# Performance work log

Measured on AMD Instinct MI355X. Metric: run time of the kernel, lower is better.

## Reference

```python
import jax, jax.numpy as jnp
import numpy as np

D = 1024      # d_model
H = 16        # heads
KD = 64       # per-head dim
STRIDE = 64   # local chunk size
LH = 8        # local heads
GH = H - LH   # global heads
C = 4         # attended positions per global head per chunk


def setup_inputs() -> dict:
    key = jax.random.key(0)
    ks = jax.random.split(key, 12)
    B, S = 4, 4096
    sc = 1.0 / np.sqrt(D)
    x = jax.random.normal(ks[0], (B, S, D), jnp.float32)
    input_mask = jax.random.randint(ks[1], (B, S), 0, 2).astype(bool)
    Wq = jax.random.normal(ks[2], (D, D), jnp.float32) * sc
    bq = jax.random.normal(ks[3], (D,), jnp.float32) * 0.01
    Wk = jax.random.normal(ks[4], (D, D), jnp.float32) * sc
    bk = jax.random.normal(ks[5], (D,), jnp.float32) * 0.01
    Wv = jax.random.normal(ks[6], (D, D), jnp.float32) * sc
    bv = jax.random.normal(ks[7], (D,), jnp.float32) * 0.01
    Wo = jax.random.normal(ks[8], (D, D), jnp.float32) * sc
    bo = jax.random.normal(ks[9], (D,), jnp.float32) * 0.01
    return {"x": x, "input_mask": input_mask, "Wq": Wq, "bq": bq,
            "Wk": Wk, "bk": bk, "Wv": Wv, "bv": bv, "Wo": Wo, "bo": bo}


def reference(x, input_mask, Wq, bq, Wk, bk, Wv, bv, Wo, bo):
    B, S, _ = x.shape
    q = (x @ Wq.T + bq).reshape(B, S, H, KD)
    k = (x @ Wk.T + bk).reshape(B, S, H, KD)
    v = (x @ Wv.T + bv).reshape(B, S, H, KD)

    # ---- local heads: per the original code, the local attention scores are
    # computed but discarded; local_qkv = chunk_local_value reshaped back,
    # which is exactly the (head-major) local values. We reproduce that math.
    local_qkv = jnp.transpose(v[:, :, :LH, :], (0, 2, 1, 3))  # (B, LH, S, KD)

    # ---- global heads: each global head attends, inside every chunk, to a
    # fixed window of C positions near the end of the chunk.
    nc = S // STRIDE
    start = STRIDE - GH * C
    base = jnp.arange(start, STRIDE).reshape(GH, C)          # (GH, C)
    offs = jnp.arange(0, S, STRIDE)                          # (nc,)
    idx = (base[:, None, :] + offs[None, :, None]).reshape(GH, nc * C)  # (GH, L)
    L = nc * C

    gq = jnp.transpose(q[:, :, LH:, :], (0, 2, 1, 3))        # (B, GH, S, KD)
    gk = jnp.transpose(k[:, :, LH:, :], (0, 2, 1, 3))
    gv = jnp.transpose(v[:, :, LH:, :], (0, 2, 1, 3))

    h_idx = jnp.arange(GH)[:, None]                          # (GH, 1)
    gk_sel = gk[:, h_idx, idx, :]                            # (B, GH, L, KD)
    gv_sel = gv[:, h_idx, idx, :]                            # (B, GH, L, KD)

    qk = jnp.einsum('bhsd,bhld->bhsl', gq, gk_sel) * (KD ** -0.5)
    gmask = input_mask[:, idx]                               # (B, GH, L)
    qk = jnp.where(gmask[:, :, None, :], jnp.float32(-1e10), qk)
    attn = jax.nn.softmax(qk, axis=-1)
    g_out = jnp.einsum('bhsl,bhld->bhsd', attn, gv_sel)      # (B, GH, S, KD)

    qkv = jnp.concatenate([local_qkv, g_out], axis=1)        # (B, H, S, KD)
    qkv = jnp.transpose(qkv, (0, 2, 1, 3)).reshape(B, S, H * KD)
    return qkv @ Wo.T + bo
```

## Files before the change

kernel.cpp:

```cpp
#include <hip/hip_runtime.h>
#include <stdint.h>


typedef __bf16 bf16_t;
typedef __bf16 bf16x4 __attribute__((ext_vector_type(4)));
typedef __bf16 bf16x8 __attribute__((ext_vector_type(8)));
typedef float floatx4 __attribute__((ext_vector_type(4)));

#define MFMA16(a, b, c) __builtin_amdgcn_mfma_f32_16x16x32_bf16((a), (b), (c), 0, 0, 0)

__device__ __forceinline__ void glds16(const bf16_t* g, const bf16_t* lds_base) {
  __builtin_amdgcn_global_load_lds(
      (const __attribute__((address_space(1))) uint32_t*)(uintptr_t)g,
      (__attribute__((address_space(3))) uint32_t*)(uintptr_t)lds_base, 16, 0, 0);
}

#define VMCNT(n)  asm volatile("s_waitcnt vmcnt(" #n ")" ::: "memory")
#define LGKMCNT0  asm volatile("s_waitcnt lgkmcnt(0)" ::: "memory")
#define SBAR      __builtin_amdgcn_s_barrier()
#define SCHED0    __builtin_amdgcn_sched_barrier(0)

__global__ void cvt_f32_bf16(const float* __restrict__ src, bf16_t* __restrict__ dst, int n) {
  const int i = (blockIdx.x * 256 + threadIdx.x) * 4;
  if (i < n) {
    float4 v = *(const float4*)(src + i);
    bf16x4 d = {(bf16_t)v.x, (bf16_t)v.y, (bf16_t)v.z, (bf16_t)v.w};
    *(bf16x4*)(dst + i) = d;
  }
}

__global__ void pack_bias(const float* __restrict__ bv, const float* __restrict__ bq,
                          const float* __restrict__ bk, float* __restrict__ bcat) {
  const int i = blockIdx.x * 256 + threadIdx.x;
  float v;
  if (i < 1024) v = bv[i];
  else if (i < 1536) v = bq[i - 512];
  else v = bk[i - 1024];
  bcat[i] = v;
}

#define G8_DECL                                                                 \
  __shared__ bf16_t As[2][16384];                                               \
  __shared__ bf16_t Bs[2][16384];                                               \
  const int tid = threadIdx.x;                                                  \
  const int w = tid >> 6, l = tid & 63;                                         \
  const int lq = l >> 4, lm = l & 15;                                           \
  const int wr = (w >> 2) << 7;                      \
  const int wc = (w & 3) << 6;                \
  floatx4 acc[8][4];                                                            \
  { floatx4 z = {0.f, 0.f, 0.f, 0.f};                                           \
    _Pragma("unroll") for (int i = 0; i < 8; ++i)                               \
    _Pragma("unroll") for (int j = 0; j < 4; ++j) acc[i][j] = z; }              \
  const int t7 = tid & 127, t8 = tid >> 7;                                      \
  const int sbase = ((((w >> 1) << 8) + ((w & 1) << 6)) << 3);

#define G8_ST_A(s, off, jk)                                                     \
  glds16(pAt + (off),         &As[s][0] + ((jk) << 13) + sbase);                \
  glds16(pAt + aoff2 + (off), &As[s][0] + ((jk) << 13) + 1024 + sbase);
#define G8_ST_B(s, off, jk)                                                     \
  glds16(pBt + (off),          &Bs[s][0] + ((jk) << 13) + sbase);               \
  glds16(pBt + 131072 + (off), &Bs[s][0] + ((jk) << 13) + 1024 + sbase);

#define G8_READ_B(s, kk)                                                        \
  _Pragma("unroll") for (int nt = 0; nt < 4; ++nt)                              \
    bfr[nt] = *(const bf16x8*)(&Bs[s][0] +                                      \
        (((((kk) * 4 + lq) << 8) + wc + nt * 16 + lm) << 3));

#define G8_READ_A(s, kk, mh)                                                    \
  _Pragma("unroll") for (int i = 0; i < 4; ++i)                                 \
    af[i] = *(const bf16x8*)(&As[s][0] +                                        \
        (((((kk) * 4 + lq) << 8) + wr + (mh) * 64 + i * 16 + lm) << 3));

#define G8_MFMA(mh)                                                             \
  __builtin_amdgcn_s_setprio(1);                                                \
  _Pragma("unroll") for (int i = 0; i < 4; ++i)                                 \
    _Pragma("unroll") for (int nt = 0; nt < 4; ++nt)                            \
      acc[(mh) * 4 + i][nt] = MFMA16(af[i], bfr[nt], acc[(mh) * 4 + i][nt]);    \
  __builtin_amdgcn_s_setprio(0);

#define PH_PRE   SCHED0; SBAR; LGKMCNT0; SCHED0;
#define PH_POST  SCHED0; SBAR; SCHED0;

#define G8_ITER                                                                 \
    G8_READ_A(0, 0, 0) G8_READ_B(0, 0)                                          \
    G8_ST_A(1, 96, 1)                                                           \
    PH_PRE G8_MFMA(0) PH_POST                                                   \
    G8_READ_A(0, 0, 1)                                                          \
    G8_ST_B(1, 96, 1)                                                           \
    VMCNT(4);                                                                   \
    PH_PRE G8_MFMA(1) PH_POST                                                   \
    G8_READ_A(0, 1, 0) G8_READ_B(0, 1)                                          \
    G8_ST_A(0, 128, 0)                                                          \
    PH_PRE G8_MFMA(0) PH_POST                                                   \
    G8_READ_A(0, 1, 1)                                                          \
    G8_ST_B(0, 128, 0)                                                          \
    PH_PRE G8_MFMA(1) PH_POST                                                   \
    G8_READ_A(1, 0, 0) G8_READ_B(1, 0)                                          \
    G8_ST_A(0, 160, 1)                                                          \
    PH_PRE G8_MFMA(0) PH_POST                                                   \
    G8_READ_A(1, 0, 1)                                                          \
    G8_ST_B(0, 160, 1)                                                          \
    VMCNT(8);                                                                   \
    PH_PRE G8_MFMA(1) PH_POST                                                   \
    G8_READ_A(1, 1, 0) G8_READ_B(1, 1)                                          \
    G8_ST_A(1, 192, 0)                                                          \
    PH_PRE G8_MFMA(0) PH_POST                                                   \
    G8_READ_A(1, 1, 1)                                                          \
    G8_ST_B(1, 192, 0)                                                          \
    VMCNT(8);                                                                   \
    PH_PRE G8_MFMA(1) PH_POST

#define G8_TAIL                                                                 \
    G8_READ_A(0, 0, 0) G8_READ_B(0, 0)                                          \
    G8_ST_A(1, 96, 1)                                                           \
    PH_PRE G8_MFMA(0) PH_POST                                                   \
    G8_READ_A(0, 0, 1)                                                          \
    G8_ST_B(1, 96, 1)                                                           \
    VMCNT(4);                                                                   \
    PH_PRE G8_MFMA(1) PH_POST                                                   \
    G8_READ_A(0, 1, 0) G8_READ_B(0, 1)                                          \
    PH_PRE G8_MFMA(0) PH_POST                                                   \
    G8_READ_A(0, 1, 1)                                                          \
    PH_PRE G8_MFMA(1) PH_POST                                                   \
    G8_READ_A(1, 0, 0) G8_READ_B(1, 0)                                          \
    PH_PRE G8_MFMA(0) PH_POST                                                   \
    G8_READ_A(1, 0, 1)                                                          \
    VMCNT(0);                                                                   \
    PH_PRE G8_MFMA(1) PH_POST                                                   \
    G8_READ_A(1, 1, 0) G8_READ_B(1, 1)                                          \
    PH_PRE G8_MFMA(0) PH_POST                                                   \
    G8_READ_A(1, 1, 1)                                                          \
    PH_PRE G8_MFMA(1) PH_POST

#define G8_MAIN                                                                 \
  G8_ST_A(0, 0, 0) G8_ST_B(0, 0, 0)                                             \
  G8_ST_A(0, 32, 1) G8_ST_B(0, 32, 1)                                           \
  G8_ST_A(1, 64, 0) G8_ST_B(1, 64, 0)                                           \
  VMCNT(0); SBAR; SCHED0;                                                       \
  bf16x8 af[4], bfr[4];                                                         \
  for (int t = 0; t < 7; ++t) {                                                 \
    G8_ITER                                                                     \
    pAt += 128; pBt += 128;                                                     \
  }                                                                             \
  G8_TAIL

__global__ __launch_bounds__(512, 2)
void gemm_fused(const bf16_t* __restrict__ A, const bf16_t* __restrict__ Wcat,
                const float* __restrict__ bcat, bf16_t* __restrict__ qkv,
                bf16_t* __restrict__ vg, bf16_t* __restrict__ qg,
                bf16_t* __restrict__ kg) {
  G8_DECL
  const int n = blockIdx.x;
  long row0, col0;
  int aoff2;
  const bf16_t* pAt;
  if (n < 256) {
    const int xcd = n & 7, j = n >> 3;
    const int ct = j >> 3;
    row0 = (long)(xcd * 8 + (j & 7)) * 256;
    col0 = ct * 256 + (ct >= 2 ? 512 : 0);
    aoff2 = 131072;
    pAt = A + (row0 + t7) * 1024 + t8 * 8;
  } else {
    const int m2 = n - 256;
    const int xcd = m2 & 7, j = m2 >> 3;
    const int ct = j >> 2;
    row0 = (long)(xcd * 4 + (j & 3)) * 256;
    col0 = (ct < 2) ? (512 + ct * 256) : (1536 + (ct - 2) * 256);
    aoff2 = 262144;
    long r = row0 + t7;
    if (r > 8063) r = 8063;
    const long g = ((r >> 5) << 6) + 32 + (r & 31);
    pAt = A + g * 1024 + t8 * 8;
  }
  const bf16_t* pBt = Wcat + (col0 + t7) * 1024 + t8 * 8;
  G8_MAIN
  bf16_t* dst; long ld, cofs;
  if (col0 < 512)       { dst = qkv; ld = 1024; cofs = 0; }
  else if (col0 < 1024) { dst = vg;  ld = 512;  cofs = 512; }
  else if (col0 < 1536) { dst = qg;  ld = 512;  cofs = 1024; }
  else                  { dst = kg;  ld = 512;  cofs = 1536; }
#pragma unroll
  for (int nt = 0; nt < 4; ++nt) {
    const long col = col0 + wc + nt * 16 + lm;
    const float bc = bcat[col];
    const long cl = col - cofs;
#pragma unroll
    for (int mt = 0; mt < 8; ++mt) {
#pragma unroll
      for (int r = 0; r < 4; ++r) {
        const long row = row0 + wr + mt * 16 + lq * 4 + r;
        dst[row * ld + cl] = (bf16_t)(acc[mt][nt][r] + bc);
      }
    }
  }
}

__global__ __launch_bounds__(512, 2)
void gemm_bt(const bf16_t* __restrict__ A, const bf16_t* __restrict__ W,
             const float* __restrict__ bias, float* __restrict__ C, int ldc) {
  G8_DECL
  const int n = blockIdx.x, xcd = n & 7, j = n >> 3;
  const long row0 = (long)(xcd * 8 + (j & 7)) * 256;
  const long col0 = (long)(j >> 3) * 256;
  const int aoff2 = 131072;
  const bf16_t* pAt = A + (row0 + t7) * 1024 + t8 * 8;
  const bf16_t* pBt = W + (col0 + t7) * 1024 + t8 * 8;
  G8_MAIN
#pragma unroll
  for (int nt = 0; nt < 4; ++nt) {
    const long col = col0 + wc + nt * 16 + lm;
    const float bc = bias[col];
#pragma unroll
    for (int mt = 0; mt < 8; ++mt) {
#pragma unroll
      for (int r = 0; r < 4; ++r) {
        const long row = row0 + wr + mt * 16 + lq * 4 + r;
        C[row * (long)ldc + col] = acc[mt][nt][r] + bc;
      }
    }
  }
}

__global__ __launch_bounds__(256, 1)
void attn_sparse(const bf16_t* __restrict__ qg, const bf16_t* __restrict__ kg,
                 const bf16_t* __restrict__ vg, const int* __restrict__ mask,
                 bf16_t* __restrict__ qkv) {
  __shared__ bf16_t Ks[16384];
  __shared__ bf16_t Vt[64 * 264];
  __shared__ bf16_t Ps[4 * 16 * 136];
  __shared__ int smask[256];

  const int tid = threadIdx.x;
  const int b = blockIdx.z, h = blockIdx.y, qt = blockIdx.x;

  {
    const int lk = tid;
    const int token = ((lk >> 2) << 6) + 32 + (h << 2) + (lk & 3);
    const int selrow = ((lk >> 2) << 5) + (h << 2) + (lk & 3);
    const size_t rowi = (size_t)(b * 2048 + selrow);
    const uint4* ksrc = (const uint4*)(kg + rowi * 512 + h * 64);
#pragma unroll
    for (int kq = 0; kq < 8; ++kq)
      *(uint4*)(Ks + (kq * 256 + lk) * 8) = ksrc[kq];
    const bf16_t* vsrc = vg + rowi * 512 + h * 64;
#pragma unroll
    for (int i = 0; i < 8; ++i) {
      bf16x8 vv = *(const bf16x8*)(vsrc + i * 8);
#pragma unroll
      for (int j = 0; j < 8; ++j) Vt[(i * 8 + j) * 264 + lk] = vv[j];
    }
    smask[lk] = mask[b * 4096 + token];
  }
  __syncthreads();

  const int w = tid >> 6, l = tid & 63, lq = l >> 4, lm = l & 15;
  const int mrow = (qt << 6) + (w << 4);

  const bf16_t* qrow = qg + (size_t)(b * 4096 + mrow + lm) * 512 + h * 64 + lq * 8;
  bf16x8 aq0 = *(const bf16x8*)qrow;
  bf16x8 aq1 = *(const bf16x8*)(qrow + 32);

  floatx4 zero4 = {0.f, 0.f, 0.f, 0.f};
  floatx4 s[16];
#pragma unroll
  for (int t = 0; t < 16; ++t) {
    bf16x8 kb0 = *(const bf16x8*)(Ks + (lq * 256 + t * 16 + lm) * 8);
    bf16x8 kb1 = *(const bf16x8*)(Ks + ((4 + lq) * 256 + t * 16 + lm) * 8);
    floatx4 z = zero4;
    z = MFMA16(aq0, kb0, z);
    z = MFMA16(aq1, kb1, z);
    s[t] = z;
  }

  float rmax[4] = {-1e30f, -1e30f, -1e30f, -1e30f};
#pragma unroll
  for (int t = 0; t < 16; ++t) {
    const bool mk = smask[t * 16 + lm] != 0;
#pragma unroll
    for (int r = 0; r < 4; ++r) {
      float v = s[t][r] * 0.125f;
      v = mk ? -1e10f : v;
      s[t][r] = v;
      rmax[r] = fmaxf(rmax[r], v);
    }
  }
#pragma unroll
  for (int off = 1; off < 16; off <<= 1)
#pragma unroll
    for (int r = 0; r < 4; ++r) rmax[r] = fmaxf(rmax[r], __shfl_xor(rmax[r], off));
  float rsum[4] = {0.f, 0.f, 0.f, 0.f};
#pragma unroll
  for (int t = 0; t < 16; ++t)
#pragma unroll
    for (int r = 0; r < 4; ++r) {
      float p = __expf(s[t][r] - rmax[r]);
      s[t][r] = p;
      rsum[r] += p;
    }
#pragma unroll
  for (int off = 1; off < 16; off <<= 1)
#pragma unroll
    for (int r = 0; r < 4; ++r) rsum[r] += __shfl_xor(rsum[r], off);
  float rinv[4];
#pragma unroll
  for (int r = 0; r < 4; ++r) rinv[r] = 1.0f / rsum[r];

  floatx4 o[4];
#pragma unroll
  for (int dt = 0; dt < 4; ++dt) o[dt] = zero4;
  bf16_t* Pw = Ps + w * (16 * 136);
#pragma unroll
  for (int half = 0; half < 2; ++half) {
#pragma unroll
    for (int t = 0; t < 8; ++t) {
      const int tt = half * 8 + t;
#pragma unroll
      for (int r = 0; r < 4; ++r)
        Pw[(lq * 4 + r) * 136 + t * 16 + lm] = (bf16_t)(s[tt][r] * rinv[r]);
    }
    __syncthreads();
#pragma unroll
    for (int ks = 0; ks < 4; ++ks) {
      bf16x8 pa = *(const bf16x8*)(Pw + lm * 136 + ks * 32 + lq * 8);
#pragma unroll
      for (int dt = 0; dt < 4; ++dt) {
        bf16x8 vb = *(const bf16x8*)(Vt + (dt * 16 + lm) * 264 + half * 128 + ks * 32 + lq * 8);
        o[dt] = MFMA16(pa, vb, o[dt]);
      }
    }
    __syncthreads();
  }

#pragma unroll
  for (int dt = 0; dt < 4; ++dt) {
    const int d = dt * 16 + lm;
#pragma unroll
    for (int r = 0; r < 4; ++r) {
      const int token = mrow + lq * 4 + r;
      qkv[(size_t)(b * 4096 + token) * 1024 + 512 + h * 64 + d] = (bf16_t)o[dt][r];
    }
  }
}

extern "C" void kernel_launch(void* const* d_in, const int* in_sizes, int n_in,
                              void* d_out, int out_size, void* d_ws, size_t ws_size,
                              hipStream_t stream) {
  const float* x   = (const float*)d_in[0];
  const int* mask  = (const int*)d_in[1];
  const float* Wq  = (const float*)d_in[2];
  const float* bq  = (const float*)d_in[3];
  const float* Wk  = (const float*)d_in[4];
  const float* bk  = (const float*)d_in[5];
  const float* Wv  = (const float*)d_in[6];
  const float* bv  = (const float*)d_in[7];
  const float* Wo  = (const float*)d_in[8];
  const float* bo  = (const float*)d_in[9];
  float* out = (float*)d_out;

  char* ws = (char*)d_ws;
  bf16_t* xb   = (bf16_t*)(ws);
  bf16_t* Wcat = (bf16_t*)(ws + 33554432L);
  bf16_t* Wob  = (bf16_t*)(ws + 37748736L);
  float*  bcat = (float*)(ws + 39845888L);
  bf16_t* vg   = (bf16_t*)(ws + 39854080L);
  bf16_t* qg   = (bf16_t*)(ws + 56631296L);
  bf16_t* kg   = (bf16_t*)(ws + 73408512L);
  bf16_t* qkv  = (bf16_t*)(ws + 90185728L);

  dim3 blk(256);
  cvt_f32_bf16<<<16384, blk, 0, stream>>>(x, xb, 16777216);
  cvt_f32_bf16<<<1024, blk, 0, stream>>>(Wv, Wcat, 1048576);
  cvt_f32_bf16<<<512, blk, 0, stream>>>(Wq + 524288, Wcat + 1048576, 524288);
  cvt_f32_bf16<<<512, blk, 0, stream>>>(Wk + 524288, Wcat + 1572864, 524288);
  cvt_f32_bf16<<<1024, blk, 0, stream>>>(Wo, Wob, 1048576);
  pack_bias<<<8, blk, 0, stream>>>(bv, bq, bk, bcat);

  gemm_fused<<<384, dim3(512), 0, stream>>>(xb, Wcat, bcat, qkv, vg, qg, kg);
  attn_sparse<<<dim3(64, 8, 4), dim3(256), 0, stream>>>(qg, kg, vg, mask, qkv);
  gemm_bt<<<256, dim3(512), 0, stream>>>(qkv, Wob, bo, out, 1024);
}
```

Measured before the change: 349.2 us.

## Process more query rows per attention block to amortize K/V staging

The sparse attention kernel now uses 512-thread blocks that loop over four groups of 128 query rows. The selected K and V tiles for a (batch, head) are therefore loaded into shared memory once per 512 queries instead of once per 64. The block-wide barriers around the per-wave P buffer are removed, since each wave only touches its own slice. The grid shrinks to 256 blocks, which reduces parallel slack and latency hiding across CUs.

```diff
diff --git a/kernel.cpp b/kernel.cpp
--- a/kernel.cpp
+++ b/kernel.cpp
@@ -222,123 +222,130 @@
   }
 }
 
-__global__ __launch_bounds__(256, 1)
+__global__ __launch_bounds__(512, 1)
 void attn_sparse(const bf16_t* __restrict__ qg, const bf16_t* __restrict__ kg,
                  const bf16_t* __restrict__ vg, const int* __restrict__ mask,
                  bf16_t* __restrict__ qkv) {
   __shared__ bf16_t Ks[16384];
   __shared__ bf16_t Vt[64 * 264];
-  __shared__ bf16_t Ps[4 * 16 * 136];
+  __shared__ bf16_t Ps[8 * 16 * 136];
   __shared__ int smask[256];
 
   const int tid = threadIdx.x;
-  const int b = blockIdx.z, h = blockIdx.y, qt = blockIdx.x;
+  const int b = blockIdx.z, h = blockIdx.y, qq = blockIdx.x;
 
   {
-    const int lk = tid;
-    const int token = ((lk >> 2) << 6) + 32 + (h << 2) + (lk & 3);
+    const int lk = tid & 255;
+    const int hf = tid >> 8;
     const int selrow = ((lk >> 2) << 5) + (h << 2) + (lk & 3);
     const size_t rowi = (size_t)(b * 2048 + selrow);
     const uint4* ksrc = (const uint4*)(kg + rowi * 512 + h * 64);
 #pragma unroll
-    for (int kq = 0; kq < 8; ++kq)
-      *(uint4*)(Ks + (kq * 256 + lk) * 8) = ksrc[kq];
+    for (int kq = 0; kq < 4; ++kq) {
+      const int kq8 = hf * 4 + kq;
+      *(uint4*)(Ks + (kq8 * 256 + lk) * 8) = ksrc[kq8];
+    }
     const bf16_t* vsrc = vg + rowi * 512 + h * 64;
 #pragma unroll
-    for (int i = 0; i < 8; ++i) {
-      bf16x8 vv = *(const bf16x8*)(vsrc + i * 8);
-#pragma unroll
-      for (int j = 0; j < 8; ++j) Vt[(i * 8 + j) * 264 + lk] = vv[j];
-    }
-    smask[lk] = mask[b * 4096 + token];
+    for (int i = 0; i < 4; ++i) {
+      const int i8 = hf * 4 + i;
+      bf16x8 vv = *(const bf16x8*)(vsrc + i8 * 8);
+#pragma unroll
+      for (int j = 0; j < 8; ++j) Vt[(i8 * 8 + j) * 264 + lk] = vv[j];
+    }
+    if (tid < 256) {
+      const int token = ((lk >> 2) << 6) + 32 + (h << 2) + (lk & 3);
+      smask[lk] = mask[b * 4096 + token];
+    }
   }
   __syncthreads();
 
   const int w = tid >> 6, l = tid & 63, lq = l >> 4, lm = l & 15;
-  const int mrow = (qt << 6) + (w << 4);
-
-  const bf16_t* qrow = qg + (size_t)(b * 4096 + mrow + lm) * 512 + h * 64 + lq * 8;
-  bf16x8 aq0 = *(const bf16x8*)qrow;
-  bf16x8 aq1 = *(const bf16x8*)(qrow + 32);
-
+  bf16_t* Pw = Ps + w * (16 * 136);
   floatx4 zero4 = {0.f, 0.f, 0.f, 0.f};
-  floatx4 s[16];
-#pragma unroll
-  for (int t = 0; t < 16; ++t) {
-    bf16x8 kb0 = *(const bf16x8*)(Ks + (lq * 256 + t * 16 + lm) * 8);
-    bf16x8 kb1 = *(const bf16x8*)(Ks + ((4 + lq) * 256 + t * 16 + lm) * 8);
-    floatx4 z = zero4;
-    z = MFMA16(aq0, kb0, z);
-    z = MFMA16(aq1, kb1, z);
-    s[t] = z;
-  }
-
-  float rmax[4] = {-1e30f, -1e30f, -1e30f, -1e30f};
-#pragma unroll
-  for (int t = 0; t < 16; ++t) {
-    const bool mk = smask[t * 16 + lm] != 0;
-#pragma unroll
-    for (int r = 0; r < 4; ++r) {
-      float v = s[t][r] * 0.125f;
-      v = mk ? -1e10f : v;
-      s[t][r] = v;
-      rmax[r] = fmaxf(rmax[r], v);
-    }
-  }
-#pragma unroll
-  for (int off = 1; off < 16; off <<= 1)
-#pragma unroll
-    for (int r = 0; r < 4; ++r) rmax[r] = fmaxf(rmax[r], __shfl_xor(rmax[r], off));
-  float rsum[4] = {0.f, 0.f, 0.f, 0.f};
-#pragma unroll
-  for (int t = 0; t < 16; ++t)
-#pragma unroll
-    for (int r = 0; r < 4; ++r) {
-      float p = __expf(s[t][r] - rmax[r]);
-      s[t][r] = p;
-      rsum[r] += p;
-    }
-#pragma unroll
-  for (int off = 1; off < 16; off <<= 1)
-#pragma unroll
-    for (int r = 0; r < 4; ++r) rsum[r] += __shfl_xor(rsum[r], off);
-  float rinv[4];
-#pragma unroll
-  for (int r = 0; r < 4; ++r) rinv[r] = 1.0f / rsum[r];
-
-  floatx4 o[4];
-#pragma unroll
-  for (int dt = 0; dt < 4; ++dt) o[dt] = zero4;
-  bf16_t* Pw = Ps + w * (16 * 136);
-#pragma unroll
-  for (int half = 0; half < 2; ++half) {
-#pragma unroll
-    for (int t = 0; t < 8; ++t) {
-      const int tt = half * 8 + t;
-#pragma unroll
-      for (int r = 0; r < 4; ++r)
-        Pw[(lq * 4 + r) * 136 + t * 16 + lm] = (bf16_t)(s[tt][r] * rinv[r]);
-    }
-    __syncthreads();
-#pragma unroll
-    for (int ks = 0; ks < 4; ++ks) {
-      bf16x8 pa = *(const bf16x8*)(Pw + lm * 136 + ks * 32 + lq * 8);
-#pragma unroll
-      for (int dt = 0; dt < 4; ++dt) {
-        bf16x8 vb = *(const bf16x8*)(Vt + (dt * 16 + lm) * 264 + half * 128 + ks * 32 + lq * 8);
-        o[dt] = MFMA16(pa, vb, o[dt]);
-      }
-    }
-    __syncthreads();
-  }
-
-#pragma unroll
-  for (int dt = 0; dt < 4; ++dt) {
-    const int d = dt * 16 + lm;
-#pragma unroll
-    for (int r = 0; r < 4; ++r) {
-      const int token = mrow + lq * 4 + r;
-      qkv[(size_t)(b * 4096 + token) * 1024 + 512 + h * 64 + d] = (bf16_t)o[dt][r];
+
+  for (int p = 0; p < 4; ++p) {
+    const int mrow = (qq << 9) + ((p * 8 + w) << 4);
+
+    const bf16_t* qrow = qg + (size_t)(b * 4096 + mrow + lm) * 512 + h * 64 + lq * 8;
+    bf16x8 aq0 = *(const bf16x8*)qrow;
+    bf16x8 aq1 = *(const bf16x8*)(qrow + 32);
+
+    floatx4 s[16];
+#pragma unroll
+    for (int t = 0; t < 16; ++t) {
+      bf16x8 kb0 = *(const bf16x8*)(Ks + (lq * 256 + t * 16 + lm) * 8);
+      bf16x8 kb1 = *(const bf16x8*)(Ks + ((4 + lq) * 256 + t * 16 + lm) * 8);
+      floatx4 z = zero4;
+      z = MFMA16(aq0, kb0, z);
+      z = MFMA16(aq1, kb1, z);
+      s[t] = z;
+    }
+
+    float rmax[4] = {-1e30f, -1e30f, -1e30f, -1e30f};
+#pragma unroll
+    for (int t = 0; t < 16; ++t) {
+      const bool mk = smask[t * 16 + lm] != 0;
+#pragma unroll
+      for (int r = 0; r < 4; ++r) {
+        float v = s[t][r] * 0.125f;
+        v = mk ? -1e10f : v;
+        s[t][r] = v;
+        rmax[r] = fmaxf(rmax[r], v);
+      }
+    }
+#pragma unroll
+    for (int off = 1; off < 16; off <<= 1)
+#pragma unroll
+      for (int r = 0; r < 4; ++r) rmax[r] = fmaxf(rmax[r], __shfl_xor(rmax[r], off));
+    float rsum[4] = {0.f, 0.f, 0.f, 0.f};
+#pragma unroll
+    for (int t = 0; t < 16; ++t)
+#pragma unroll
+      for (int r = 0; r < 4; ++r) {
+        float pp = __expf(s[t][r] - rmax[r]);
+        s[t][r] = pp;
+        rsum[r] += pp;
+      }
+#pragma unroll
+    for (int off = 1; off < 16; off <<= 1)
+#pragma unroll
+      for (int r = 0; r < 4; ++r) rsum[r] += __shfl_xor(rsum[r], off);
+    float rinv[4];
+#pragma unroll
+    for (int r = 0; r < 4; ++r) rinv[r] = 1.0f / rsum[r];
+
+    floatx4 o[4];
+#pragma unroll
+    for (int dt = 0; dt < 4; ++dt) o[dt] = zero4;
+#pragma unroll
+    for (int half = 0; half < 2; ++half) {
+#pragma unroll
+      for (int t = 0; t < 8; ++t) {
+        const int tt = half * 8 + t;
+#pragma unroll
+        for (int r = 0; r < 4; ++r)
+          Pw[(lq * 4 + r) * 136 + t * 16 + lm] = (bf16_t)(s[tt][r] * rinv[r]);
+      }
+#pragma unroll
+      for (int ks = 0; ks < 4; ++ks) {
+        bf16x8 pa = *(const bf16x8*)(Pw + lm * 136 + ks * 32 + lq * 8);
+#pragma unroll
+        for (int dt = 0; dt < 4; ++dt) {
+          bf16x8 vb = *(const bf16x8*)(Vt + (dt * 16 + lm) * 264 + half * 128 + ks * 32 + lq * 8);
+          o[dt] = MFMA16(pa, vb, o[dt]);
+        }
+      }
+    }
+
+#pragma unroll
+    for (int dt = 0; dt < 4; ++dt) {
+      const int d = dt * 16 + lm;
+#pragma unroll
+      for (int r = 0; r < 4; ++r) {
+        const int token = mrow + lq * 4 + r;
+        qkv[(size_t)(b * 4096 + token) * 1024 + 512 + h * 64 + d] = (bf16_t)o[dt][r];
+      }
     }
   }
 }
@@ -377,6 +384,6 @@
   pack_bias<<<8, blk, 0, stream>>>(bv, bq, bk, bcat);
 
   gemm_fused<<<384, dim3(512), 0, stream>>>(xb, Wcat, bcat, qkv, vg, qg, kg);
-  attn_sparse<<<dim3(64, 8, 4), dim3(256), 0, stream>>>(qg, kg, vg, mask, qkv);
+  attn_sparse<<<dim3(8, 8, 4), dim3(512), 0, stream>>>(qg, kg, vg, mask, qkv);
   gemm_bt<<<256, dim3(512), 0, stream>>>(qkv, Wob, bo, out, 1024);
 }
```

Result: faster. 320.8 us (-8.1%).
